# Kernel tuning notes

Measured on AMD Instinct MI355X. Metric: run time of the kernel, lower is better.

The kernel has to match this reference:

```python
import jax, jax.numpy as jnp
import numpy as np

N_NODES = 50000
N_EDGES = 600000
DIM = 128
NUM_CLASSES = 10
EPS = 1e-15
MAX_NORM = 1.0 - 1e-5  # keep points strictly inside the unit ball for artanh


def _norm(x):
    return jnp.maximum(jnp.linalg.norm(x, axis=-1, keepdims=True), EPS)


def logmap0(x):
    # Poincare ball, c=1: artanh(||x||) * x / ||x||
    n = _norm(x)
    return jnp.arctanh(jnp.minimum(n, MAX_NORM)) * x / n


def expmap0(u):
    # Poincare ball, c=1: tanh(||u||) * u / ||u||
    n = _norm(u)
    return jnp.tanh(n) * u / n


def hyp_conv(x, W, b, src, dst):
    t = logmap0(x)                       # [N, D] manifold -> tangent at origin
    h = t @ W.T + b                      # [N, D] linear in tangent space
    y = expmap0(h)                       # [N, D] back to manifold
    # message passing: gather source features, scatter-add at destinations
    return jax.ops.segment_sum(y[src], dst, num_segments=N_NODES)


def setup_inputs() -> dict:
    key = jax.random.key(0)
    ks = jax.random.split(key, 8)
    edge_index = jax.random.randint(ks[0], (2, N_EDGES), 0, N_NODES, dtype=jnp.int64)
    # entity embeddings: small tangent vectors mapped onto the ball
    x = expmap0(0.01 * jax.random.normal(ks[1], (N_NODES, DIM), dtype=jnp.float32))
    s = 1.0 / np.sqrt(DIM)
    W1 = jax.random.normal(ks[2], (DIM, DIM), dtype=jnp.float32) * s
    b1 = jax.random.normal(ks[3], (DIM,), dtype=jnp.float32) * 0.01
    W2 = jax.random.normal(ks[4], (DIM, DIM), dtype=jnp.float32) * s
    b2 = jax.random.normal(ks[5], (DIM,), dtype=jnp.float32) * 0.01
    Wc = jax.random.normal(ks[6], (NUM_CLASSES, DIM), dtype=jnp.float32) * s
    bc = jax.random.normal(ks[7], (NUM_CLASSES,), dtype=jnp.float32) * 0.01
    return {"edge_index": edge_index, "x": x, "W1": W1, "b1": b1,
            "W2": W2, "b2": b2, "Wc": Wc, "bc": bc}


def reference(edge_index, x, W1, b1, W2, b2, Wc, bc):
    src, dst = edge_index[0], edge_index[1]
    h = hyp_conv(x, W1, b1, src, dst)
    h = jax.nn.relu(h)
    h = hyp_conv(h, W2, b2, src, dst)
    h = jax.nn.relu(h)
    t = logmap0(h)
    return t @ Wc.T + bc  # [N_NODES, NUM_CLASSES]
```

## Files before the change

### kernel.cpp

```cpp
#include <hip/hip_runtime.h>

#define N_NODES 50000
#define N_EDGES 600000
#define DIM 128
#define NCLS 10
#define ELLW 64
#define EPSF 1e-15f
#define MAXNORM 0.99999f
#define NTILE ((N_NODES + 63) / 64)

typedef __attribute__((ext_vector_type(8))) short bf16x8;
typedef __attribute__((ext_vector_type(4))) float f32x4;

__device__ inline float waveSum(float v) {
#pragma unroll
  for (int o = 1; o < 64; o <<= 1) v += __shfl_xor(v, o, 64);
  return v;
}

__device__ inline unsigned short f2bf(float f) {
  union { float f; unsigned u; } c; c.f = f;
  return (unsigned short)((c.u + 0x7FFFu + ((c.u >> 16) & 1u)) >> 16);
}
__device__ inline float bf_lo(unsigned u) {
  union { unsigned u; float f; } c; c.u = u << 16; return c.f;
}
__device__ inline float bf_hi(unsigned u) {
  union { unsigned u; float f; } c; c.u = u & 0xFFFF0000u; return c.f;
}

__global__ __launch_bounds__(256) void init_kernel(
    int* __restrict__ cursor, const float* __restrict__ W1, const float* __restrict__ W2,
    unsigned short* __restrict__ W1b, unsigned short* __restrict__ W2b)
{
  int i = blockIdx.x * 256 + threadIdx.x;
  if (i < N_NODES) cursor[i] = 0;
  if (i < DIM * DIM) {
    W1b[i] = f2bf(W1[i]);
    W2b[i] = f2bf(W2[i]);
  }
}

__global__ __launch_bounds__(256) void fill_kernel(
    const int* __restrict__ src, const int* __restrict__ dst,
    int* __restrict__ cursor, int* __restrict__ ell)
{
  int e = blockIdx.x * 256 + threadIdx.x;
  if (e < N_EDGES) {
    int d = dst[e];
    int slot = atomicAdd(&cursor[d], 1);
    ell[d * ELLW + slot] = src[e];
  }
}

__global__ __launch_bounds__(256) void gatherT_kernel(
    const unsigned short* __restrict__ y, const int* __restrict__ cursor,
    const int* __restrict__ ell, unsigned short* __restrict__ tout)
{
  const int node = blockIdx.x * 4 + (threadIdx.x >> 6);
  if (node >= N_NODES) return;
  const int lane = threadIdx.x & 63;
  const int* lst = ell + node * ELLW;
  const int cnt = cursor[node];
  float2 a0 = {0.f, 0.f}, a1 = {0.f, 0.f}, a2 = {0.f, 0.f}, a3 = {0.f, 0.f};
  int j = 0;
  for (; j + 7 < cnt; j += 8) {
    unsigned u0 = ((const unsigned*)(y + (size_t)lst[j    ] * DIM))[lane];
    unsigned u1 = ((const unsigned*)(y + (size_t)lst[j + 1] * DIM))[lane];
    unsigned u2 = ((const unsigned*)(y + (size_t)lst[j + 2] * DIM))[lane];
    unsigned u3 = ((const unsigned*)(y + (size_t)lst[j + 3] * DIM))[lane];
    unsigned u4 = ((const unsigned*)(y + (size_t)lst[j + 4] * DIM))[lane];
    unsigned u5 = ((const unsigned*)(y + (size_t)lst[j + 5] * DIM))[lane];
    unsigned u6 = ((const unsigned*)(y + (size_t)lst[j + 6] * DIM))[lane];
    unsigned u7 = ((const unsigned*)(y + (size_t)lst[j + 7] * DIM))[lane];
    a0.x += bf_lo(u0); a0.y += bf_hi(u0);
    a1.x += bf_lo(u1); a1.y += bf_hi(u1);
    a2.x += bf_lo(u2); a2.y += bf_hi(u2);
    a3.x += bf_lo(u3); a3.y += bf_hi(u3);
    a0.x += bf_lo(u4); a0.y += bf_hi(u4);
    a1.x += bf_lo(u5); a1.y += bf_hi(u5);
    a2.x += bf_lo(u6); a2.y += bf_hi(u6);
    a3.x += bf_lo(u7); a3.y += bf_hi(u7);
  }
  for (; j + 3 < cnt; j += 4) {
    unsigned u0 = ((const unsigned*)(y + (size_t)lst[j    ] * DIM))[lane];
    unsigned u1 = ((const unsigned*)(y + (size_t)lst[j + 1] * DIM))[lane];
    unsigned u2 = ((const unsigned*)(y + (size_t)lst[j + 2] * DIM))[lane];
    unsigned u3 = ((const unsigned*)(y + (size_t)lst[j + 3] * DIM))[lane];
    a0.x += bf_lo(u0); a0.y += bf_hi(u0);
    a1.x += bf_lo(u1); a1.y += bf_hi(u1);
    a2.x += bf_lo(u2); a2.y += bf_hi(u2);
    a3.x += bf_lo(u3); a3.y += bf_hi(u3);
  }
  for (; j < cnt; ++j) {
    unsigned u0 = ((const unsigned*)(y + (size_t)lst[j] * DIM))[lane];
    a0.x += bf_lo(u0); a0.y += bf_hi(u0);
  }
  float2 r;
  r.x = fmaxf((a0.x + a1.x) + (a2.x + a3.x), 0.f);
  r.y = fmaxf((a0.y + a1.y) + (a2.y + a3.y), 0.f);

  float s = waveSum(r.x * r.x + r.y * r.y);
  float n = sqrtf(s);
  float nc = fmaxf(n, EPSF);
  float nm = fminf(nc, MAXNORM);
  float scale = 0.5f * logf((1.0f + nm) / (1.0f - nm)) / nc;
  unsigned u = (unsigned)f2bf(r.x * scale) | ((unsigned)f2bf(r.y * scale) << 16);
  ((unsigned*)(tout + (size_t)node * DIM))[lane] = u;
}

template <int MODE>
__global__ __launch_bounds__(256, 2) void transform_mfma(
    const void* __restrict__ xin, const unsigned short* __restrict__ Wb,
    const float* __restrict__ b, unsigned short* __restrict__ y)
{
  const int tid = threadIdx.x;
  const int w = tid >> 6;
  const int l = tid & 63;
  const int lr = l & 15;
  const int lg = l >> 4;

  __shared__ __align__(16) unsigned short At[64 * DIM];

  bf16x8 bf[8][4];
#pragma unroll
  for (int n = 0; n < 8; ++n)
#pragma unroll
    for (int kc = 0; kc < 4; ++kc)
      bf[n][kc] = *(const bf16x8*)(Wb + (n * 16 + lr) * DIM + kc * 32 + lg * 8);

  float bias[8];
#pragma unroll
  for (int n = 0; n < 8; ++n) bias[n] = b[n * 16 + lr];

  const int row = w * 16 + lr;

  for (int tile = blockIdx.x; tile < NTILE; tile += gridDim.x) {
    const int base = tile * 64;
    const int node = base + row;
    __syncthreads();

    if (MODE == 0) {
      const float* x = (const float*)xin;
      float v[32];
      if (node < N_NODES) {
        const float4* xr = (const float4*)(x + (size_t)node * DIM + lg * 32);
#pragma unroll
        for (int q = 0; q < 8; ++q) {
          float4 f = xr[q];
          v[q * 4 + 0] = f.x; v[q * 4 + 1] = f.y; v[q * 4 + 2] = f.z; v[q * 4 + 3] = f.w;
        }
      } else {
#pragma unroll
        for (int q = 0; q < 32; ++q) v[q] = 0.f;
      }
      float sq = 0.f;
#pragma unroll
      for (int q = 0; q < 32; ++q) sq += v[q] * v[q];
      sq += __shfl_xor(sq, 16, 64);
      sq += __shfl_xor(sq, 32, 64);
      float n1 = sqrtf(sq);
      float nc = fmaxf(n1, EPSF);
      float nm = fminf(nc, MAXNORM);
      float scale = 0.5f * logf((1.f + nm) / (1.f - nm)) / nc;
#pragma unroll
      for (int s = 0; s < 4; ++s) {
        unsigned short tmp[8];
#pragma unroll
        for (int e = 0; e < 8; ++e) tmp[e] = f2bf(v[s * 8 + e] * scale);
        int byte = row * 256 + lg * 64 + s * 16;
        byte ^= (row & 7) << 4;
        *(bf16x8*)((char*)At + byte) = *(const bf16x8*)tmp;
      }
    } else {
      const unsigned short* t = (const unsigned short*)xin;
#pragma unroll
      for (int s = 0; s < 4; ++s) {
        bf16x8 frag;
        if (node < N_NODES)
          frag = *(const bf16x8*)(t + (size_t)node * DIM + lg * 32 + s * 8);
        else
          frag = bf16x8{0, 0, 0, 0, 0, 0, 0, 0};
        int byte = row * 256 + lg * 64 + s * 16;
        byte ^= (row & 7) << 4;
        *(bf16x8*)((char*)At + byte) = frag;
      }
    }
    __syncthreads();

    f32x4 acc[8];
#pragma unroll
    for (int n = 0; n < 8; ++n) {
      acc[n][0] = bias[n]; acc[n][1] = bias[n]; acc[n][2] = bias[n]; acc[n][3] = bias[n];
    }
#pragma unroll
    for (int kc = 0; kc < 4; ++kc) {
      int arow = w * 16 + lr;
      int byte = arow * 256 + kc * 64 + lg * 16;
      byte ^= (arow & 7) << 4;
      bf16x8 af = *(const bf16x8*)((const char*)At + byte);
#pragma unroll
      for (int n = 0; n < 8; ++n)
        acc[n] = __builtin_amdgcn_mfma_f32_16x16x32_bf16(af, bf[n][kc], acc[n], 0, 0, 0);
    }

    float rs[4];
#pragma unroll
    for (int j = 0; j < 4; ++j) {
      float s2 = 0.f;
#pragma unroll
      for (int n = 0; n < 8; ++n) s2 += acc[n][j] * acc[n][j];
      s2 += __shfl_xor(s2, 1, 64);
      s2 += __shfl_xor(s2, 2, 64);
      s2 += __shfl_xor(s2, 4, 64);
      s2 += __shfl_xor(s2, 8, 64);
      float n2 = sqrtf(s2);
      float n2c = fmaxf(n2, EPSF);
      rs[j] = tanhf(n2c) / n2c;
    }
#pragma unroll
    for (int j = 0; j < 4; ++j) {
      int nrow = base + w * 16 + lg * 4 + j;
      if (nrow < N_NODES) {
        unsigned short* yr = y + (size_t)nrow * DIM + lr;
#pragma unroll
        for (int n = 0; n < 8; ++n) yr[n * 16] = f2bf(acc[n][j] * rs[j]);
      }
    }
  }
}

__global__ __launch_bounds__(256) void head_mfma(
    const unsigned short* __restrict__ t2, const float* __restrict__ Wc,
    const float* __restrict__ bc, float* __restrict__ out)
{
  const int base = blockIdx.x * 64;
  const int w = threadIdx.x >> 6;
  const int l = threadIdx.x & 63;
  const int lr = l & 15;
  const int lg = l >> 4;

  bf16x8 bw[4];
#pragma unroll
  for (int kc = 0; kc < 4; ++kc) {
    unsigned short tmp[8];
    if (lr < NCLS) {
      const float* wr = Wc + (size_t)lr * DIM + kc * 32 + lg * 8;
#pragma unroll
      for (int e = 0; e < 8; ++e) tmp[e] = f2bf(wr[e]);
    } else {
#pragma unroll
      for (int e = 0; e < 8; ++e) tmp[e] = 0;
    }
    bw[kc] = *(const bf16x8*)tmp;
  }
  const float bias = (lr < NCLS) ? bc[lr] : 0.f;

  const int arow = base + w * 16 + lr;
  f32x4 acc;
  acc[0] = bias; acc[1] = bias; acc[2] = bias; acc[3] = bias;
#pragma unroll
  for (int kc = 0; kc < 4; ++kc) {
    bf16x8 af;
    if (arow < N_NODES)
      af = *(const bf16x8*)(t2 + (size_t)arow * DIM + kc * 32 + lg * 8);
    else
      af = bf16x8{0, 0, 0, 0, 0, 0, 0, 0};
    acc = __builtin_amdgcn_mfma_f32_16x16x32_bf16(af, bw[kc], acc, 0, 0, 0);
  }

  if (lr < NCLS) {
#pragma unroll
    for (int j = 0; j < 4; ++j) {
      int nrow = base + w * 16 + lg * 4 + j;
      if (nrow < N_NODES) out[(size_t)nrow * NCLS + lr] = acc[j];
    }
  }
}

extern "C" void kernel_launch(void* const* d_in, const int* in_sizes, int n_in,
                              void* d_out, int out_size, void* d_ws, size_t ws_size,
                              hipStream_t stream)
{
  const int* edge = (const int*)d_in[0];
  const int* src = edge;
  const int* dst = edge + N_EDGES;
  const float* x  = (const float*)d_in[1];
  const float* W1 = (const float*)d_in[2];
  const float* b1 = (const float*)d_in[3];
  const float* W2 = (const float*)d_in[4];
  const float* b2 = (const float*)d_in[5];
  const float* Wc = (const float*)d_in[6];
  const float* bc = (const float*)d_in[7];
  float* out = (float*)d_out;

  unsigned short* ybuf = (unsigned short*)d_ws;
  unsigned short* tbuf = ybuf + (size_t)N_NODES * DIM;
  unsigned short* W1b = tbuf + (size_t)N_NODES * DIM;
  unsigned short* W2b = W1b + DIM * DIM;
  int* cursor = (int*)(W2b + DIM * DIM);
  int* ell    = cursor + N_NODES;

  init_kernel<<<(N_NODES + 255) / 256, 256, 0, stream>>>(cursor, W1, W2, W1b, W2b);

  fill_kernel<<<(N_EDGES + 255) / 256, 256, 0, stream>>>(src, dst, cursor, ell);

  transform_mfma<0><<<512, 256, 0, stream>>>(x, W1b, b1, ybuf);
  gatherT_kernel<<<(N_NODES + 3) / 4, 256, 0, stream>>>(ybuf, cursor, ell, tbuf);

  transform_mfma<1><<<512, 256, 0, stream>>>(tbuf, W2b, b2, ybuf);
  gatherT_kernel<<<(N_NODES + 3) / 4, 256, 0, stream>>>(ybuf, cursor, ell, tbuf);

  head_mfma<<<NTILE, 256, 0, stream>>>(tbuf, Wc, bc, out);
}
```

Before: 151.8 us.

## Merge ELL fill and first transform into one launch; pad cursors against contention

The edge-to-ELL fill and the first layer's MFMA transform are independent, so they now run as disjoint block ranges of a single kernel and overlap. Each fill thread handles four edges with batched loads and atomics to expose more memory parallelism. Per-node cursors are padded to a 16-int stride so atomics on neighbouring nodes land on separate cache lines. This adds workspace for the padded cursors and gives the fused kernel the MFMA kernel's register and LDS footprint.

```diff
diff --git a/kernel.cpp b/kernel.cpp
--- a/kernel.cpp
+++ b/kernel.cpp
@@ -5,9 +5,12 @@
 #define DIM 128
 #define NCLS 10
 #define ELLW 64
+#define CURSTRIDE 16
 #define EPSF 1e-15f
 #define MAXNORM 0.99999f
 #define NTILE ((N_NODES + 63) / 64)
+#define FILL_BLOCKS 586
+#define XFORM_BLOCKS 512
 
 typedef __attribute__((ext_vector_type(8))) short bf16x8;
 typedef __attribute__((ext_vector_type(4))) float f32x4;
@@ -34,22 +37,137 @@
     unsigned short* __restrict__ W1b, unsigned short* __restrict__ W2b)
 {
   int i = blockIdx.x * 256 + threadIdx.x;
-  if (i < N_NODES) cursor[i] = 0;
+  if (i < N_NODES) cursor[i * CURSTRIDE] = 0;
   if (i < DIM * DIM) {
     W1b[i] = f2bf(W1[i]);
     W2b[i] = f2bf(W2[i]);
   }
 }
 
-__global__ __launch_bounds__(256) void fill_kernel(
+__global__ __launch_bounds__(256, 2) void fill_transform(
     const int* __restrict__ src, const int* __restrict__ dst,
-    int* __restrict__ cursor, int* __restrict__ ell)
-{
-  int e = blockIdx.x * 256 + threadIdx.x;
-  if (e < N_EDGES) {
-    int d = dst[e];
-    int slot = atomicAdd(&cursor[d], 1);
-    ell[d * ELLW + slot] = src[e];
+    int* __restrict__ cursor, int* __restrict__ ell,
+    const float* __restrict__ x, const unsigned short* __restrict__ Wb,
+    const float* __restrict__ b, unsigned short* __restrict__ y)
+{
+  __shared__ __align__(16) unsigned short At[64 * DIM];
+
+  if (blockIdx.x < FILL_BLOCKS) {
+    const int nthr = FILL_BLOCKS * 256;
+    const int e = blockIdx.x * 256 + threadIdx.x;
+    const int e0 = e, e1 = e + nthr, e2 = e + 2 * nthr, e3 = e + 3 * nthr;
+    int d0, d1, d2, d3, s0, s1, s2, s3;
+    if (e0 < N_EDGES) { d0 = dst[e0]; s0 = src[e0]; }
+    if (e1 < N_EDGES) { d1 = dst[e1]; s1 = src[e1]; }
+    if (e2 < N_EDGES) { d2 = dst[e2]; s2 = src[e2]; }
+    if (e3 < N_EDGES) { d3 = dst[e3]; s3 = src[e3]; }
+    int p0, p1, p2, p3;
+    if (e0 < N_EDGES) p0 = atomicAdd(&cursor[d0 * CURSTRIDE], 1);
+    if (e1 < N_EDGES) p1 = atomicAdd(&cursor[d1 * CURSTRIDE], 1);
+    if (e2 < N_EDGES) p2 = atomicAdd(&cursor[d2 * CURSTRIDE], 1);
+    if (e3 < N_EDGES) p3 = atomicAdd(&cursor[d3 * CURSTRIDE], 1);
+    if (e0 < N_EDGES) ell[d0 * ELLW + p0] = s0;
+    if (e1 < N_EDGES) ell[d1 * ELLW + p1] = s1;
+    if (e2 < N_EDGES) ell[d2 * ELLW + p2] = s2;
+    if (e3 < N_EDGES) ell[d3 * ELLW + p3] = s3;
+    return;
+  }
+
+  const int tid = threadIdx.x;
+  const int w = tid >> 6;
+  const int l = tid & 63;
+  const int lr = l & 15;
+  const int lg = l >> 4;
+
+  bf16x8 bf[8][4];
+#pragma unroll
+  for (int n = 0; n < 8; ++n)
+#pragma unroll
+    for (int kc = 0; kc < 4; ++kc)
+      bf[n][kc] = *(const bf16x8*)(Wb + (n * 16 + lr) * DIM + kc * 32 + lg * 8);
+
+  float bias[8];
+#pragma unroll
+  for (int n = 0; n < 8; ++n) bias[n] = b[n * 16 + lr];
+
+  const int row = w * 16 + lr;
+
+  for (int tile = blockIdx.x - FILL_BLOCKS; tile < NTILE; tile += XFORM_BLOCKS) {
+    const int base = tile * 64;
+    const int node = base + row;
+    __syncthreads();
+
+    float v[32];
+    if (node < N_NODES) {
+      const float4* xr = (const float4*)(x + (size_t)node * DIM + lg * 32);
+#pragma unroll
+      for (int q = 0; q < 8; ++q) {
+        float4 f = xr[q];
+        v[q * 4 + 0] = f.x; v[q * 4 + 1] = f.y; v[q * 4 + 2] = f.z; v[q * 4 + 3] = f.w;
+      }
+    } else {
+#pragma unroll
+      for (int q = 0; q < 32; ++q) v[q] = 0.f;
+    }
+    float sq = 0.f;
+#pragma unroll
+    for (int q = 0; q < 32; ++q) sq += v[q] * v[q];
+    sq += __shfl_xor(sq, 16, 64);
+    sq += __shfl_xor(sq, 32, 64);
+    float n1 = sqrtf(sq);
+    float nc = fmaxf(n1, EPSF);
+    float nm = fminf(nc, MAXNORM);
+    float scale = 0.5f * logf((1.f + nm) / (1.f - nm)) / nc;
+#pragma unroll
+    for (int s = 0; s < 4; ++s) {
+      unsigned short tmp[8];
+#pragma unroll
+      for (int e = 0; e < 8; ++e) tmp[e] = f2bf(v[s * 8 + e] * scale);
+      int byte = row * 256 + lg * 64 + s * 16;
+      byte ^= (row & 7) << 4;
+      *(bf16x8*)((char*)At + byte) = *(const bf16x8*)tmp;
+    }
+    __syncthreads();
+
+    f32x4 acc[8];
+#pragma unroll
+    for (int n = 0; n < 8; ++n) {
+      acc[n][0] = bias[n]; acc[n][1] = bias[n]; acc[n][2] = bias[n]; acc[n][3] = bias[n];
+    }
+#pragma unroll
+    for (int kc = 0; kc < 4; ++kc) {
+      int arow = w * 16 + lr;
+      int byte = arow * 256 + kc * 64 + lg * 16;
+      byte ^= (arow & 7) << 4;
+      bf16x8 af = *(const bf16x8*)((const char*)At + byte);
+#pragma unroll
+      for (int n = 0; n < 8; ++n)
+        acc[n] = __builtin_amdgcn_mfma_f32_16x16x32_bf16(af, bf[n][kc], acc[n], 0, 0, 0);
+    }
+
+    float rs[4];
+#pragma unroll
+    for (int j = 0; j < 4; ++j) {
+      float s2 = 0.f;
+#pragma unroll
+      for (int n = 0; n < 8; ++n) s2 += acc[n][j] * acc[n][j];
+      s2 += __shfl_xor(s2, 1, 64);
+      s2 += __shfl_xor(s2, 2, 64);
+      s2 += __shfl_xor(s2, 4, 64);
+      s2 += __shfl_xor(s2, 8, 64);
+      float n2 = sqrtf(s2);
+      float n2c = fmaxf(n2, EPSF);
+      rs[j] = tanhf(n2c) / n2c;
+    }
+#pragma unroll
+    for (int j = 0; j < 4; ++j) {
+      int nrow = base + w * 16 + lg * 4 + j;
+      if (nrow < N_NODES) {
+        unsigned short* yr = y + (size_t)nrow * DIM + lr;
+#pragma unroll
+        for (int n = 0; n < 8; ++n) yr[n * 16] = f2bf(acc[n][j] * rs[j]);
+      }
+    }
   }
 }
 
@@ -61,7 +179,7 @@
   if (node >= N_NODES) return;
   const int lane = threadIdx.x & 63;
   const int* lst = ell + node * ELLW;
-  const int cnt = cursor[node];
+  const int cnt = cursor[node * CURSTRIDE];
   float2 a0 = {0.f, 0.f}, a1 = {0.f, 0.f}, a2 = {0.f, 0.f}, a3 = {0.f, 0.f};
   int j = 0;
   for (; j + 7 < cnt; j += 8) {
@@ -109,9 +227,8 @@
   ((unsigned*)(tout + (size_t)node * DIM))[lane] = u;
 }
 
-template <int MODE>
-__global__ __launch_bounds__(256, 2) void transform_mfma(
-    const void* __restrict__ xin, const unsigned short* __restrict__ Wb,
+__global__ __launch_bounds__(256, 2) void transform2_mfma(
+    const unsigned short* __restrict__ t, const unsigned short* __restrict__ Wb,
     const float* __restrict__ b, unsigned short* __restrict__ y)
 {
   const int tid = threadIdx.x;
@@ -140,51 +257,16 @@
     const int node = base + row;
     __syncthreads();
 
-    if (MODE == 0) {
-      const float* x = (const float*)xin;
-      float v[32];
-      if (node < N_NODES) {
-        const float4* xr = (const float4*)(x + (size_t)node * DIM + lg * 32);
-#pragma unroll
-        for (int q = 0; q < 8; ++q) {
-          float4 f = xr[q];
-          v[q * 4 + 0] = f.x; v[q * 4 + 1] = f.y; v[q * 4 + 2] = f.z; v[q * 4 + 3] = f.w;
-        }
-      } else {
-#pragma unroll
-        for (int q = 0; q < 32; ++q) v[q] = 0.f;
-      }
-      float sq = 0.f;
-#pragma unroll
-      for (int q = 0; q < 32; ++q) sq += v[q] * v[q];
-      sq += __shfl_xor(sq, 16, 64);
-      sq += __shfl_xor(sq, 32, 64);
-      float n1 = sqrtf(sq);
-      float nc = fmaxf(n1, EPSF);
-      float nm = fminf(nc, MAXNORM);
-      float scale = 0.5f * logf((1.f + nm) / (1.f - nm)) / nc;
-#pragma unroll
-      for (int s = 0; s < 4; ++s) {
-        unsigned short tmp[8];
-#pragma unroll
-        for (int e = 0; e < 8; ++e) tmp[e] = f2bf(v[s * 8 + e] * scale);
-        int byte = row * 256 + lg * 64 + s * 16;
-        byte ^= (row & 7) << 4;
-        *(bf16x8*)((char*)At + byte) = *(const bf16x8*)tmp;
-      }
-    } else {
-      const unsigned short* t = (const unsigned short*)xin;
-#pragma unroll
-      for (int s = 0; s < 4; ++s) {
-        bf16x8 frag;
-        if (node < N_NODES)
-          frag = *(const bf16x8*)(t + (size_t)node * DIM + lg * 32 + s * 8);
-        else
-          frag = bf16x8{0, 0, 0, 0, 0, 0, 0, 0};
-        int byte = row * 256 + lg * 64 + s * 16;
-        byte ^= (row & 7) << 4;
-        *(bf16x8*)((char*)At + byte) = frag;
-      }
+#pragma unroll
+    for (int s = 0; s < 4; ++s) {
+      bf16x8 frag;
+      if (node < N_NODES)
+        frag = *(const bf16x8*)(t + (size_t)node * DIM + lg * 32 + s * 8);
+      else
+        frag = bf16x8{0, 0, 0, 0, 0, 0, 0, 0};
+      int byte = row * 256 + lg * 64 + s * 16;
+      byte ^= (row & 7) << 4;
+      *(bf16x8*)((char*)At + byte) = frag;
     }
     __syncthreads();
 
@@ -299,16 +381,17 @@
   unsigned short* W1b = tbuf + (size_t)N_NODES * DIM;
   unsigned short* W2b = W1b + DIM * DIM;
   int* cursor = (int*)(W2b + DIM * DIM);
-  int* ell    = cursor + N_NODES;
+  int* ell    = cursor + (size_t)N_NODES * CURSTRIDE;
 
   init_kernel<<<(N_NODES + 255) / 256, 256, 0, stream>>>(cursor, W1, W2, W1b, W2b);
 
-  fill_kernel<<<(N_EDGES + 255) / 256, 256, 0, stream>>>(src, dst, cursor, ell);
-
-  transform_mfma<0><<<512, 256, 0, stream>>>(x, W1b, b1, ybuf);
+  fill_transform<<<FILL_BLOCKS + XFORM_BLOCKS, 256, 0, stream>>>(
+      src, dst, cursor, ell, x, W1b, b1, ybuf);
+
   gatherT_kernel<<<(N_NODES + 3) / 4, 256, 0, stream>>>(ybuf, cursor, ell, tbuf);
 
-  transform_mfma<1><<<512, 256, 0, stream>>>(tbuf, W2b, b2, ybuf);
+  transform2_mfma<<<512, 256, 0, stream>>>(tbuf, W2b, b2, ybuf);
+
   gatherT_kernel<<<(N_NODES + 3) / 4, 256, 0, stream>>>(ybuf, cursor, ell, tbuf);
 
   head_mfma<<<NTILE, 256, 0, stream>>>(tbuf, Wc, bc, out);
```

New measurement: 135.9 us. 1.12x faster.

## Split node range and fuse independent stages into combined kernels for overlap

Applied to the files above, without the earlier changes.

Splits the node range at a fixed boundary so each launch can pair independent work: fill for the first half with the first transform, fill for the second half with gathering the first half, gathering the second half with transforming the first half, and so on. The cursor array is padded to one counter per 64 bytes to reduce atomic contention, and each fill thread handles four edges. A separate y2 buffer is added so the second transform does not overwrite data still being read. The goal is to remove launch gaps and idle tails between dependent stages. The block counts and split point are hand-tuned constants, and correctness depends on the stage ordering being exactly right.

```diff
diff --git a/kernel.cpp b/kernel.cpp
--- a/kernel.cpp
+++ b/kernel.cpp
@@ -5,9 +5,16 @@
 #define DIM 128
 #define NCLS 10
 #define ELLW 64
+#define CURSTRIDE 16
 #define EPSF 1e-15f
 #define MAXNORM 0.99999f
-#define NTILE ((N_NODES + 63) / 64)
+#define NTILE 782
+#define SPLIT 30784
+#define STILE 481
+#define GA_BLKS 7696
+#define GB_BLKS 4804
+#define FILLB 586
+#define XFB 512
 
 typedef __attribute__((ext_vector_type(8))) short bf16x8;
 typedef __attribute__((ext_vector_type(4))) float f32x4;
@@ -29,39 +36,163 @@
   union { unsigned u; float f; } c; c.u = u & 0xFFFF0000u; return c.f;
 }
 
-__global__ __launch_bounds__(256) void init_kernel(
-    int* __restrict__ cursor, const float* __restrict__ W1, const float* __restrict__ W2,
-    unsigned short* __restrict__ W1b, unsigned short* __restrict__ W2b)
-{
-  int i = blockIdx.x * 256 + threadIdx.x;
-  if (i < N_NODES) cursor[i] = 0;
-  if (i < DIM * DIM) {
-    W1b[i] = f2bf(W1[i]);
-    W2b[i] = f2bf(W2[i]);
-  }
-}
-
-__global__ __launch_bounds__(256) void fill_kernel(
+__device__ __forceinline__ void do_fill(
     const int* __restrict__ src, const int* __restrict__ dst,
-    int* __restrict__ cursor, int* __restrict__ ell)
-{
-  int e = blockIdx.x * 256 + threadIdx.x;
-  if (e < N_EDGES) {
-    int d = dst[e];
-    int slot = atomicAdd(&cursor[d], 1);
-    ell[d * ELLW + slot] = src[e];
-  }
-}
-
-__global__ __launch_bounds__(256) void gatherT_kernel(
+    int* __restrict__ cursor, int* __restrict__ ell,
+    int blkid, int dstLo, int dstHi)
+{
+  const int nthr = FILLB * 256;
+  const int e = blkid * 256 + (int)threadIdx.x;
+  const int e0 = e, e1 = e + nthr, e2 = e + 2 * nthr, e3 = e + 3 * nthr;
+  int d0 = -1, d1 = -1, d2 = -1, d3 = -1, s0, s1, s2, s3;
+  if (e0 < N_EDGES) { d0 = dst[e0]; s0 = src[e0]; }
+  if (e1 < N_EDGES) { d1 = dst[e1]; s1 = src[e1]; }
+  if (e2 < N_EDGES) { d2 = dst[e2]; s2 = src[e2]; }
+  if (e3 < N_EDGES) { d3 = dst[e3]; s3 = src[e3]; }
+  bool k0 = (d0 >= dstLo) & (d0 < dstHi);
+  bool k1 = (d1 >= dstLo) & (d1 < dstHi);
+  bool k2 = (d2 >= dstLo) & (d2 < dstHi);
+  bool k3 = (d3 >= dstLo) & (d3 < dstHi);
+  int p0, p1, p2, p3;
+  if (k0) p0 = atomicAdd(&cursor[d0 * CURSTRIDE], 1);
+  if (k1) p1 = atomicAdd(&cursor[d1 * CURSTRIDE], 1);
+  if (k2) p2 = atomicAdd(&cursor[d2 * CURSTRIDE], 1);
+  if (k3) p3 = atomicAdd(&cursor[d3 * CURSTRIDE], 1);
+  if (k0) ell[d0 * ELLW + p0] = s0;
+  if (k1) ell[d1 * ELLW + p1] = s1;
+  if (k2) ell[d2 * ELLW + p2] = s2;
+  if (k3) ell[d3 * ELLW + p3] = s3;
+}
+
+template <int MODE>
+__device__ __forceinline__ void do_transform(
+    const void* __restrict__ xin, const unsigned short* __restrict__ Wb,
+    const float* __restrict__ b, unsigned short* __restrict__ y,
+    unsigned short* At, int t0, int t1, int tstep)
+{
+  const int tid = threadIdx.x;
+  const int w = tid >> 6;
+  const int l = tid & 63;
+  const int lr = l & 15;
+  const int lg = l >> 4;
+
+  bf16x8 bf[8][4];
+#pragma unroll
+  for (int n = 0; n < 8; ++n)
+#pragma unroll
+    for (int kc = 0; kc < 4; ++kc)
+      bf[n][kc] = *(const bf16x8*)(Wb + (n * 16 + lr) * DIM + kc * 32 + lg * 8);
+
+  float bias[8];
+#pragma unroll
+  for (int n = 0; n < 8; ++n) bias[n] = b[n * 16 + lr];
+
+  const int row = w * 16 + lr;
+
+  for (int tile = t0; tile < t1; tile += tstep) {
+    const int base = tile * 64;
+    const int node = base + row;
+    __syncthreads();
+
+    if (MODE == 0) {
+      const float* x = (const float*)xin;
+      float v[32];
+      if (node < N_NODES) {
+        const float4* xr = (const float4*)(x + (size_t)node * DIM + lg * 32);
+#pragma unroll
+        for (int q = 0; q < 8; ++q) {
+          float4 f = xr[q];
+          v[q * 4 + 0] = f.x; v[q * 4 + 1] = f.y; v[q * 4 + 2] = f.z; v[q * 4 + 3] = f.w;
+        }
+      } else {
+#pragma unroll
+        for (int q = 0; q < 32; ++q) v[q] = 0.f;
+      }
+      float sq = 0.f;
+#pragma unroll
+      for (int q = 0; q < 32; ++q) sq += v[q] * v[q];
+      sq += __shfl_xor(sq, 16, 64);
+      sq += __shfl_xor(sq, 32, 64);
+      float n1 = sqrtf(sq);
+      float nc = fmaxf(n1, EPSF);
+      float nm = fminf(nc, MAXNORM);
+      float scale = 0.5f * logf((1.f + nm) / (1.f - nm)) / nc;
+#pragma unroll
+      for (int s = 0; s < 4; ++s) {
+        unsigned short tmp[8];
+#pragma unroll
+        for (int e = 0; e < 8; ++e) tmp[e] = f2bf(v[s * 8 + e] * scale);
+        int byte = row * 256 + lg * 64 + s * 16;
+        byte ^= (row & 7) << 4;
+        *(bf16x8*)((char*)At + byte) = *(const bf16x8*)tmp;
+      }
+    } else {
+      const unsigned short* t = (const unsigned short*)xin;
+#pragma unroll
+      for (int s = 0; s < 4; ++s) {
+        bf16x8 frag;
+        if (node < N_NODES)
+          frag = *(const bf16x8*)(t + (size_t)node * DIM + lg * 32 + s * 8);
+        else
+          frag = bf16x8{0, 0, 0, 0, 0, 0, 0, 0};
+        int byte = row * 256 + lg * 64 + s * 16;
+        byte ^= (row & 7) << 4;
+        *(bf16x8*)((char*)At + byte) = frag;
+      }
+    }
+    __syncthreads();
+
+    f32x4 acc[8];
+#pragma unroll
+    for (int n = 0; n < 8; ++n) {
+      acc[n][0] = bias[n]; acc[n][1] = bias[n]; acc[n][2] = bias[n]; acc[n][3] = bias[n];
+    }
+#pragma unroll
+    for (int kc = 0; kc < 4; ++kc) {
+      int byte = row * 256 + kc * 64 + lg * 16;
+      byte ^= (row & 7) << 4;
+      bf16x8 af = *(const bf16x8*)((const char*)At + byte);
+#pragma unroll
+      for (int n = 0; n < 8; ++n)
+        acc[n] = __builtin_amdgcn_mfma_f32_16x16x32_bf16(af, bf[n][kc], acc[n], 0, 0, 0);
+    }
+
+    float rs[4];
+#pragma unroll
+    for (int j = 0; j < 4; ++j) {
+      float s2 = 0.f;
+#pragma unroll
+      for (int n = 0; n < 8; ++n) s2 += acc[n][j] * acc[n][j];
+      s2 += __shfl_xor(s2, 1, 64);
+      s2 += __shfl_xor(s2, 2, 64);
+      s2 += __shfl_xor(s2, 4, 64);
+      s2 += __shfl_xor(s2, 8, 64);
+      float n2 = sqrtf(s2);
+      float n2c = fmaxf(n2, EPSF);
+      rs[j] = tanhf(n2c) / n2c;
+    }
+#pragma unroll
+    for (int j = 0; j < 4; ++j) {
+      int nrow = base + w * 16 + lg * 4 + j;
+      if (nrow < N_NODES) {
+        unsigned short* yr = y + (size_t)nrow * DIM + lr;
+#pragma unroll
+        for (int n = 0; n < 8; ++n) yr[n * 16] = f2bf(acc[n][j] * rs[j]);
+      }
+    }
+  }
+}
+
+__device__ __forceinline__ void do_gather(
     const unsigned short* __restrict__ y, const int* __restrict__ cursor,
-    const int* __restrict__ ell, unsigned short* __restrict__ tout)
-{
-  const int node = blockIdx.x * 4 + (threadIdx.x >> 6);
-  if (node >= N_NODES) return;
+    const int* __restrict__ ell, unsigned short* __restrict__ tout,
+    int blkid, int nodeLo, int nodeHi)
+{
+  const int node = nodeLo + blkid * 4 + ((int)threadIdx.x >> 6);
+  if (node >= nodeHi) return;
   const int lane = threadIdx.x & 63;
-  const int* lst = ell + node * ELLW;
-  const int cnt = cursor[node];
+  const int* lst = ell + (size_t)node * ELLW;
+  const int cnt = cursor[node * CURSTRIDE];
   float2 a0 = {0.f, 0.f}, a1 = {0.f, 0.f}, a2 = {0.f, 0.f}, a3 = {0.f, 0.f};
   int j = 0;
   for (; j + 7 < cnt; j += 8) {
@@ -109,133 +240,12 @@
   ((unsigned*)(tout + (size_t)node * DIM))[lane] = u;
 }
 
-template <int MODE>
-__global__ __launch_bounds__(256, 2) void transform_mfma(
-    const void* __restrict__ xin, const unsigned short* __restrict__ Wb,
-    const float* __restrict__ b, unsigned short* __restrict__ y)
-{
-  const int tid = threadIdx.x;
-  const int w = tid >> 6;
-  const int l = tid & 63;
-  const int lr = l & 15;
-  const int lg = l >> 4;
-
-  __shared__ __align__(16) unsigned short At[64 * DIM];
-
-  bf16x8 bf[8][4];
-#pragma unroll
-  for (int n = 0; n < 8; ++n)
-#pragma unroll
-    for (int kc = 0; kc < 4; ++kc)
-      bf[n][kc] = *(const bf16x8*)(Wb + (n * 16 + lr) * DIM + kc * 32 + lg * 8);
-
-  float bias[8];
-#pragma unroll
-  for (int n = 0; n < 8; ++n) bias[n] = b[n * 16 + lr];
-
-  const int row = w * 16 + lr;
-
-  for (int tile = blockIdx.x; tile < NTILE; tile += gridDim.x) {
-    const int base = tile * 64;
-    const int node = base + row;
-    __syncthreads();
-
-    if (MODE == 0) {
-      const float* x = (const float*)xin;
-      float v[32];
-      if (node < N_NODES) {
-        const float4* xr = (const float4*)(x + (size_t)node * DIM + lg * 32);
-#pragma unroll
-        for (int q = 0; q < 8; ++q) {
-          float4 f = xr[q];
-          v[q * 4 + 0] = f.x; v[q * 4 + 1] = f.y; v[q * 4 + 2] = f.z; v[q * 4 + 3] = f.w;
-        }
-      } else {
-#pragma unroll
-        for (int q = 0; q < 32; ++q) v[q] = 0.f;
-      }
-      float sq = 0.f;
-#pragma unroll
-      for (int q = 0; q < 32; ++q) sq += v[q] * v[q];
-      sq += __shfl_xor(sq, 16, 64);
-      sq += __shfl_xor(sq, 32, 64);
-      float n1 = sqrtf(sq);
-      float nc = fmaxf(n1, EPSF);
-      float nm = fminf(nc, MAXNORM);
-      float scale = 0.5f * logf((1.f + nm) / (1.f - nm)) / nc;
-#pragma unroll
-      for (int s = 0; s < 4; ++s) {
-        unsigned short tmp[8];
-#pragma unroll
-        for (int e = 0; e < 8; ++e) tmp[e] = f2bf(v[s * 8 + e] * scale);
-        int byte = row * 256 + lg * 64 + s * 16;
-        byte ^= (row & 7) << 4;
-        *(bf16x8*)((char*)At + byte) = *(const bf16x8*)tmp;
-      }
-    } else {
-      const unsigned short* t = (const unsigned short*)xin;
-#pragma unroll
-      for (int s = 0; s < 4; ++s) {
-        bf16x8 frag;
-        if (node < N_NODES)
-          frag = *(const bf16x8*)(t + (size_t)node * DIM + lg * 32 + s * 8);
-        else
-          frag = bf16x8{0, 0, 0, 0, 0, 0, 0, 0};
-        int byte = row * 256 + lg * 64 + s * 16;
-        byte ^= (row & 7) << 4;
-        *(bf16x8*)((char*)At + byte) = frag;
-      }
-    }
-    __syncthreads();
-
-    f32x4 acc[8];
-#pragma unroll
-    for (int n = 0; n < 8; ++n) {
-      acc[n][0] = bias[n]; acc[n][1] = bias[n]; acc[n][2] = bias[n]; acc[n][3] = bias[n];
-    }
-#pragma unroll
-    for (int kc = 0; kc < 4; ++kc) {
-      int arow = w * 16 + lr;
-      int byte = arow * 256 + kc * 64 + lg * 16;
-      byte ^= (arow & 7) << 4;
-      bf16x8 af = *(const bf16x8*)((const char*)At + byte);
-#pragma unroll
-      for (int n = 0; n < 8; ++n)
-        acc[n] = __builtin_amdgcn_mfma_f32_16x16x32_bf16(af, bf[n][kc], acc[n], 0, 0, 0);
-    }
-
-    float rs[4];
-#pragma unroll
-    for (int j = 0; j < 4; ++j) {
-      float s2 = 0.f;
-#pragma unroll
-      for (int n = 0; n < 8; ++n) s2 += acc[n][j] * acc[n][j];
-      s2 += __shfl_xor(s2, 1, 64);
-      s2 += __shfl_xor(s2, 2, 64);
-      s2 += __shfl_xor(s2, 4, 64);
-      s2 += __shfl_xor(s2, 8, 64);
-      float n2 = sqrtf(s2);
-      float n2c = fmaxf(n2, EPSF);
-      rs[j] = tanhf(n2c) / n2c;
-    }
-#pragma unroll
-    for (int j = 0; j < 4; ++j) {
-      int nrow = base + w * 16 + lg * 4 + j;
-      if (nrow < N_NODES) {
-        unsigned short* yr = y + (size_t)nrow * DIM + lr;
-#pragma unroll
-        for (int n = 0; n < 8; ++n) yr[n * 16] = f2bf(acc[n][j] * rs[j]);
-      }
-    }
-  }
-}
-
-__global__ __launch_bounds__(256) void head_mfma(
+__device__ __forceinline__ void do_head(
     const unsigned short* __restrict__ t2, const float* __restrict__ Wc,
-    const float* __restrict__ bc, float* __restrict__ out)
-{
-  const int base = blockIdx.x * 64;
-  const int w = threadIdx.x >> 6;
+    const float* __restrict__ bc, float* __restrict__ out, int tile)
+{
+  const int base = tile * 64;
+  const int w = (int)threadIdx.x >> 6;
   const int l = threadIdx.x & 63;
   const int lr = l & 15;
   const int lg = l >> 4;
@@ -276,6 +286,97 @@
       if (nrow < N_NODES) out[(size_t)nrow * NCLS + lr] = acc[j];
     }
   }
+}
+
+
+__global__ __launch_bounds__(256) void k_init(
+    int* __restrict__ cursor, const float* __restrict__ W1, const float* __restrict__ W2,
+    unsigned short* __restrict__ W1b, unsigned short* __restrict__ W2b)
+{
+  int i = blockIdx.x * 256 + threadIdx.x;
+  if (i < N_NODES) cursor[i * CURSTRIDE] = 0;
+  if (i < DIM * DIM) {
+    W1b[i] = f2bf(W1[i]);
+    W2b[i] = f2bf(W2[i]);
+  }
+}
+
+__global__ __launch_bounds__(256, 3) void k_fillA_t1(
+    const int* __restrict__ src, const int* __restrict__ dst,
+    int* __restrict__ cursor, int* __restrict__ ell,
+    const float* __restrict__ x, const unsigned short* __restrict__ W1b,
+    const float* __restrict__ b1, unsigned short* __restrict__ y)
+{
+  __shared__ __align__(16) unsigned short At[64 * DIM];
+  if (blockIdx.x < FILLB) {
+    do_fill(src, dst, cursor, ell, blockIdx.x, 0, SPLIT);
+  } else {
+    int lb = blockIdx.x - FILLB;
+    do_transform<0>(x, W1b, b1, y, At, lb, NTILE, XFB);
+  }
+}
+
+__global__ __launch_bounds__(256) void k_fillB_g1A(
+    const int* __restrict__ src, const int* __restrict__ dst,
+    int* __restrict__ cursor, int* __restrict__ ell,
+    const unsigned short* __restrict__ y, unsigned short* __restrict__ t)
+{
+  if (blockIdx.x < FILLB) {
+    do_fill(src, dst, cursor, ell, blockIdx.x, SPLIT, N_NODES);
+  } else {
+    do_gather(y, cursor, ell, t, blockIdx.x - FILLB, 0, SPLIT);
+  }
+}
+
+__global__ __launch_bounds__(256, 3) void k_g1B_t2A(
+    const unsigned short* __restrict__ y, const int* __restrict__ cursor,
+    const int* __restrict__ ell, unsigned short* __restrict__ t,
+    const unsigned short* __restrict__ W2b, const float* __restrict__ b2,
+    unsigned short* __restrict__ y2)
+{
+  __shared__ __align__(16) unsigned short At[64 * DIM];
+  if (blockIdx.x < GB_BLKS) {
+    do_gather(y, cursor, ell, t, blockIdx.x, SPLIT, N_NODES);
+  } else {
+    int tile = blockIdx.x - GB_BLKS;
+    do_transform<1>(t, W2b, b2, y2, At, tile, tile + 1, 1);
+  }
+}
+
+__global__ __launch_bounds__(256, 3) void k_t2B(
+    const unsigned short* __restrict__ t, const unsigned short* __restrict__ W2b,
+    const float* __restrict__ b2, unsigned short* __restrict__ y2)
+{
+  __shared__ __align__(16) unsigned short At[64 * DIM];
+  int tile = STILE + blockIdx.x;
+  do_transform<1>(t, W2b, b2, y2, At, tile, tile + 1, 1);
+}
+
+__global__ __launch_bounds__(256) void k_g2A(
+    const unsigned short* __restrict__ y2, const int* __restrict__ cursor,
+    const int* __restrict__ ell, unsigned short* __restrict__ t2)
+{
+  do_gather(y2, cursor, ell, t2, blockIdx.x, 0, SPLIT);
+}
+
+__global__ __launch_bounds__(256) void k_g2B_headA(
+    const unsigned short* __restrict__ y2, const int* __restrict__ cursor,
+    const int* __restrict__ ell, unsigned short* __restrict__ t2,
+    const float* __restrict__ Wc, const float* __restrict__ bc,
+    float* __restrict__ out)
+{
+  if (blockIdx.x < GB_BLKS) {
+    do_gather(y2, cursor, ell, t2, blockIdx.x, SPLIT, N_NODES);
+  } else {
+    do_head(t2, Wc, bc, out, blockIdx.x - GB_BLKS);
+  }
+}
+
+__global__ __launch_bounds__(256) void k_headB(
+    const unsigned short* __restrict__ t2, const float* __restrict__ Wc,
+    const float* __restrict__ bc, float* __restrict__ out)
+{
+  do_head(t2, Wc, bc, out, STILE + blockIdx.x);
 }
 
 extern "C" void kernel_launch(void* const* d_in, const int* in_sizes, int n_in,
@@ -294,22 +395,27 @@
   const float* bc = (const float*)d_in[7];
   float* out = (float*)d_out;
 
-  unsigned short* ybuf = (unsigned short*)d_ws;
-  unsigned short* tbuf = ybuf + (size_t)N_NODES * DIM;
-  unsigned short* W1b = tbuf + (size_t)N_NODES * DIM;
+  unsigned short* ybuf  = (unsigned short*)d_ws;
+  unsigned short* tbuf  = ybuf + (size_t)N_NODES * DIM;
+  unsigned short* y2buf = tbuf + (size_t)N_NODES * DIM;
+  unsigned short* W1b = y2buf + (size_t)N_NODES * DIM;
   unsigned short* W2b = W1b + DIM * DIM;
   int* cursor = (int*)(W2b + DIM * DIM);
-  int* ell    = cursor + N_NODES;
-
-  init_kernel<<<(N_NODES + 255) / 256, 256, 0, stream>>>(cursor, W1, W2, W1b, W2b);
-
-  fill_kernel<<<(N_EDGES + 255) / 256, 256, 0, stream>>>(src, dst, cursor, ell);
-
-  transform_mfma<0><<<512, 256, 0, stream>>>(x, W1b, b1, ybuf);
-  gatherT_kernel<<<(N_NODES + 3) / 4, 256, 0, stream>>>(ybuf, cursor, ell, tbuf);
-
-  transform_mfma<1><<<512, 256, 0, stream>>>(tbuf, W2b, b2, ybuf);
-  gatherT_kernel<<<(N_NODES + 3) / 4, 256, 0, stream>>>(ybuf, cursor, ell, tbuf);
-
-  head_mfma<<<NTILE, 256, 0, stream>>>(tbuf, Wc, bc, out);
-}
+  int* ell = cursor + (size_t)N_NODES * CURSTRIDE;
+
+  k_init<<<(N_NODES + 255) / 256, 256, 0, stream>>>(cursor, W1, W2, W1b, W2b);
+
+  k_fillA_t1<<<FILLB + XFB, 256, 0, stream>>>(src, dst, cursor, ell, x, W1b, b1, ybuf);
+
+  k_fillB_g1A<<<FILLB + GA_BLKS, 256, 0, stream>>>(src, dst, cursor, ell, ybuf, tbuf);
+
+  k_g1B_t2A<<<GB_BLKS + STILE, 256, 0, stream>>>(ybuf, cursor, ell, tbuf, W2b, b2, y2buf);
+
+  k_t2B<<<NTILE - STILE, 256, 0, stream>>>(tbuf, W2b, b2, y2buf);
+
+  k_g2A<<<GA_BLKS, 256, 0, stream>>>(y2buf, cursor, ell, tbuf);
+
+  k_g2B_headA<<<GB_BLKS + STILE, 256, 0, stream>>>(y2buf, cursor, ell, tbuf, Wc, bc, out);
+
+  k_headB<<<NTILE - STILE, 256, 0, stream>>>(tbuf, Wc, bc, out);
+}
```

Measured after the change: 179.1 us. +18.0%, slower.
